# Kernel tuning notes

Hardware: AMD Instinct MI355X
Metric: run time of the kernel (lower is better)

The kernel has to match this reference:

```python
import jax, jax.numpy as jnp
import numpy as np

EPS = 1e-08

def setup_inputs() -> dict:
    key = jax.random.key(0)
    k1, k2, k3 = jax.random.split(key, 3)
    b, cin, cout, ksz, h, w = 16, 256, 256, 3, 64, 64
    return {
        "x": jax.random.normal(k1, (b, cin, h, w), dtype=jnp.float32),
        "s": jax.random.normal(k2, (b, cin), dtype=jnp.float32),
        "weight": jax.random.normal(k3, (cout, cin, ksz, ksz), dtype=jnp.float32),
    }

def reference(x, s, weight):
    # x: [b, cin, h, w]; s: [b, cin]; weight: [cout, cin, k, k]
    b, cin, h, w = x.shape
    cout, _, ksz, _ = weight.shape
    pad = ksz // 2
    # demodulate pre-normalization of weight and style
    wn = weight * jax.lax.rsqrt(jnp.mean(jnp.square(weight), axis=(1, 2, 3), keepdims=True))
    sn = s * jax.lax.rsqrt(jnp.mean(jnp.square(s)))
    # per-sample modulation: [b, cout, cin, k, k]
    wmod = wn[None, :, :, :, :] * sn[:, None, :, None, None]
    # demodulation: normalize each output filter per sample
    sigma_inv = jax.lax.rsqrt(jnp.sum(jnp.square(wmod), axis=(2, 3, 4), keepdims=True) + EPS)
    wmod = wmod * sigma_inv
    # batch-grouped conv: input [1, b*cin, h, w], weight [b*cout, cin, k, k]
    xg = x.reshape(1, b * cin, h, w)
    wg = wmod.reshape(b * cout, cin, ksz, ksz)
    y = jax.lax.conv_general_dilated(
        xg, wg,
        window_strides=(1, 1),
        padding=[(pad, pad), (pad, pad)],
        feature_group_count=b,
        dimension_numbers=("NCHW", "OIHW", "NCHW"),
    )
    return y.reshape(b, cout, h, w)
```

## Files before the change

### kernel.cpp

```cpp
#include <hip/hip_runtime.h>
#include <hip/hip_bf16.h>

#define EPS 1e-8f
#define B_  16
#define CIN 256
#define COUT 256
#define HW 64

typedef __bf16 bf16x8 __attribute__((ext_vector_type(8)));
typedef float  f32x4  __attribute__((ext_vector_type(4)));

__device__ __forceinline__ void async16(void* lds, const void* g) {
    __builtin_amdgcn_global_load_lds(
        (const __attribute__((address_space(1))) unsigned int*)g,
        (__attribute__((address_space(3))) unsigned int*)lds,
        16, 0, 0);
}

__device__ __forceinline__ uint pack2(float lo, float hi) {
    __bf16 a = (__bf16)lo, b = (__bf16)hi;
    unsigned short ua = __builtin_bit_cast(unsigned short, a);
    unsigned short ub = __builtin_bit_cast(unsigned short, b);
    return ((uint)ub << 16) | (uint)ua;
}

__global__ __launch_bounds__(256) void prep_kernel(const float* __restrict__ x,
                                                   const float* __restrict__ s,
                                                   const float* __restrict__ w,
                                                   __bf16* __restrict__ xbf,
                                                   __bf16* __restrict__ wfull,
                                                   __bf16* __restrict__ zrow) {
    __shared__ uint xsd[64 * 160];
    __shared__ float red[8];
    const int bid = blockIdx.x;
    const int t   = threadIdx.x;

    if (bid == 1024) {
        uint4 z = make_uint4(0, 0, 0, 0);
        uint4* zp = (uint4*)zrow;
#pragma unroll
        for (int k = 0; k < 9; ++k) zp[k * 256 + t] = z;
        return;
    }

    if (bid > 1024) {
        const int co = bid - 1025;
        const int ci = t;
        const int lane = t & 63, wid = t >> 6;
        float as = 0.f;
#pragma unroll
        for (int k = 0; k < 16; ++k) { float sv = s[k * 256 + t]; as += sv * sv; }
        const float* wp = w + ((size_t)co * CIN + ci) * 9;
        float wv[9];
        float q = 0.f;
#pragma unroll
        for (int tp = 0; tp < 9; ++tp) { wv[tp] = wp[tp]; q += wv[tp] * wv[tp]; }
        float a = as, qq = q;
        for (int off = 32; off > 0; off >>= 1) {
            a  += __shfl_down(a,  off, 64);
            qq += __shfl_down(qq, off, 64);
        }
        if (lane == 0) { red[wid] = a; red[4 + wid] = qq; }
        __syncthreads();
        const float ssum = red[0] + red[1] + red[2] + red[3];
        const float Sw   = red[4] + red[5] + red[6] + red[7];
        const float sn2  = (float)(B_ * CIN) / ssum;
        const float wn   = rsqrtf(Sw / 2304.f);
        const float wn2sn2 = wn * wn * sn2;
        const float wsn  = wn * sqrtf(sn2);

        for (int b = 0; b < B_; ++b) {
            const float sv = s[b * CIN + ci];
            float v = sv * sv * q;
            for (int off = 32; off > 0; off >>= 1) v += __shfl_down(v, off, 64);
            __syncthreads();
            if (lane == 0) red[wid] = v;
            __syncthreads();
            const float S = red[0] + red[1] + red[2] + red[3];
            const float coef = wsn * rsqrtf(wn2sn2 * S + EPS);
            const float sc = sv * coef;
            const size_t obase = ((size_t)b * 9) * 65536 + (size_t)(ci >> 5) * 8192
                               + (size_t)co * 32 + (ci & 31);
#pragma unroll
            for (int tap = 0; tap < 9; ++tap)
                wfull[obase + (size_t)tap * 65536] = (__bf16)(wv[tap] * sc);
        }
        return;
    }

    const int row = bid & 63;
    const int b   = bid >> 6;
    const float* xbase = x + ((size_t)b * CIN * HW + row) * HW;
#pragma unroll
    for (int k = 0; k < 8; ++k) {
        int p   = k * 256 + t;
        int ci2 = p >> 4;
        int c4  = (p & 15) * 4;
        const float* src = xbase + (size_t)(2 * ci2) * (HW * HW) + c4;
        float4 v0 = *(const float4*)src;
        float4 v1 = *(const float4*)(src + HW * HW);
        const int dj = ci2 + (ci2 >> 2);
#pragma unroll
        for (int i = 0; i < 4; ++i)
            xsd[(c4 + i) * 160 + dj] = pack2((&v0.x)[i], (&v1.x)[i]);
    }
    __syncthreads();
    __bf16* orow = xbf + (((size_t)b * HW + row) * 64) * CIN;
#pragma unroll
    for (int k = 0; k < 8; ++k) {
        int o   = k * 256 + t;
        int col = o >> 5;
        int u   = o & 31;
        const uint* rp = &xsd[col * 160 + 5 * u];
        uint4 vv; vv.x = rp[0]; vv.y = rp[1]; vv.z = rp[2]; vv.w = rp[3];
        *(uint4*)&orow[(size_t)col * CIN + u * 8] = vv;
    }
}

__global__ __launch_bounds__(256, 2) void conv_mfma4(const __bf16* __restrict__ xbf,
                                                     const __bf16* __restrict__ zrow,
                                                     const __bf16* __restrict__ wfull,
                                                     float* __restrict__ out) {
    __shared__ __attribute__((aligned(16))) __bf16 xs[2][1056 * 8];

    const int bid = blockIdx.x;
    const int b   = (bid & 7) + ((bid >= 256) ? 8 : 0);
    const int r0  = ((bid >> 3) & 31) * 2;
    const int t = threadIdx.x;
    const int wy = t >> 6, lane = t & 63;
    const int m16 = lane & 15, q = lane >> 4;

    const __bf16* gsrc[5];
#pragma unroll
    for (int i = 0; i < 5; ++i) {
        int qq, rem;
        if (i < 4) { qq = i;  rem = t; }
        else       { qq = wy; rem = 256 + (lane & 7); }
        int irow = rem / 66;
        int col  = rem - irow * 66;
        int gr   = r0 - 1 + irow;
        if ((unsigned)gr < 64u && col != 0 && col != 65)
            gsrc[i] = xbf + (((size_t)b * HW + gr) * 64 + (col - 1)) * CIN + qq * 8;
        else
            gsrc[i] = zrow + col * CIN + qq * 8;
    }

#pragma unroll
    for (int i = 0; i < 4; ++i)
        async16((char*)xs[0] + (i * 264 + t) * 16, gsrc[i]);
    if (lane < 8)
        async16((char*)xs[0] + (wy * 264 + 256 + lane) * 16, gsrc[4]);

    f32x4 acc[4][8] = {};
    const __bf16* abase = wfull + (size_t)b * 589824
                        + (size_t)(wy * 64 + m16) * 32 + q * 8;

    bf16x8 afc[4];
#pragma unroll
    for (int i = 0; i < 4; ++i)
        afc[i] = *(const bf16x8*)(abase + i * 512);

    for (int cc = 0; cc < 8; ++cc) {
        const __bf16* wb = abase + (size_t)cc * 8192;
        __syncthreads();
        if (cc < 7) {
            const int d = cc * 32 + 32;
#pragma unroll
            for (int i = 0; i < 4; ++i)
                async16((char*)xs[(cc + 1) & 1] + (i * 264 + t) * 16, gsrc[i] + d);
            if (lane < 8)
                async16((char*)xs[(cc + 1) & 1] + (wy * 264 + 256 + lane) * 16, gsrc[4] + d);
        }
        const __bf16* xcur = xs[cc & 1];
#pragma unroll
        for (int tap = 0; tap < 9; ++tap) {
            const int dr = tap / 3, dc = tap % 3;
            bf16x8 bfr[8];
#pragma unroll
            for (int j = 0; j < 8; ++j) {
                const int slot = q * 264 + ((j >> 2) + dr) * 66 + (j & 3) * 16 + m16 + dc;
                bfr[j] = *(const bf16x8*)&xcur[slot * 8];
            }
            bf16x8 afn[4];
            if (tap < 8) {
#pragma unroll
                for (int i = 0; i < 4; ++i)
                    afn[i] = *(const bf16x8*)(wb + (size_t)(tap + 1) * 65536 + i * 512);
            } else if (cc < 7) {
#pragma unroll
                for (int i = 0; i < 4; ++i)
                    afn[i] = *(const bf16x8*)(wb + 8192 + i * 512);
            }
            __builtin_amdgcn_s_setprio(1);
#pragma unroll
            for (int i = 0; i < 4; ++i)
#pragma unroll
                for (int j = 0; j < 8; ++j)
                    acc[i][j] = __builtin_amdgcn_mfma_f32_16x16x32_bf16(afc[i], bfr[j], acc[i][j], 0, 0, 0);
            __builtin_amdgcn_s_setprio(0);
            if (tap < 8 || cc < 7) {
#pragma unroll
                for (int i = 0; i < 4; ++i) afc[i] = afn[i];
            }
        }
    }

#pragma unroll
    for (int i = 0; i < 4; ++i) {
        const int cobase = wy * 64 + i * 16 + q * 4;
#pragma unroll
        for (int reg = 0; reg < 4; ++reg) {
            float* op = out + ((size_t)b * COUT + (cobase + reg)) * (HW * HW) + r0 * HW + m16;
#pragma unroll
            for (int j = 0; j < 8; ++j)
                op[(j >> 2) * HW + (j & 3) * 16] = acc[i][j][reg];
        }
    }
}

extern "C" void kernel_launch(void* const* d_in, const int* in_sizes, int n_in,
                              void* d_out, int out_size, void* d_ws, size_t ws_size,
                              hipStream_t stream) {
    const float* x = (const float*)d_in[0];
    const float* s = (const float*)d_in[1];
    const float* w = (const float*)d_in[2];
    float* out = (float*)d_out;

    float* ws = (float*)d_ws;
    __bf16* wfull = (__bf16*)(ws + 70656);
    __bf16* zrow  = (__bf16*)(ws + 4789248);
    __bf16* xbf   = (__bf16*)(ws + 4798464);

    prep_kernel<<<1281, 256, 0, stream>>>(x, s, w, xbf, wfull, zrow);
    conv_mfma4<<<512, 256, 0, stream>>>(xbf, zrow, wfull, out);
}
```

Baseline: 181.1 us.

## Reuse overlapping conv rows across taps, pad LDS, and use nontemporal loads/stores

```diff
diff --git a/kernel.cpp b/kernel.cpp
--- a/kernel.cpp
+++ b/kernel.cpp
@@ -15,6 +15,12 @@
         (const __attribute__((address_space(1))) unsigned int*)g,
         (__attribute__((address_space(3))) unsigned int*)lds,
         16, 0, 0);
+}
+__device__ __forceinline__ void async16nt(void* lds, const void* g) {
+    __builtin_amdgcn_global_load_lds(
+        (const __attribute__((address_space(1))) unsigned int*)g,
+        (__attribute__((address_space(3))) unsigned int*)lds,
+        16, 0, 2);
 }
 
 __device__ __forceinline__ uint pack2(float lo, float hi) {
@@ -117,11 +123,11 @@
     }
 }
 
-__global__ __launch_bounds__(256, 2) void conv_mfma4(const __bf16* __restrict__ xbf,
+__global__ __launch_bounds__(256, 2) void conv_mfma5(const __bf16* __restrict__ xbf,
                                                      const __bf16* __restrict__ zrow,
                                                      const __bf16* __restrict__ wfull,
                                                      float* __restrict__ out) {
-    __shared__ __attribute__((aligned(16))) __bf16 xs[2][1056 * 8];
+    __shared__ __attribute__((aligned(16))) __bf16 xs[2][1064 * 8];
 
     const int bid = blockIdx.x;
     const int b   = (bid & 7) + ((bid >= 256) ? 8 : 0);
@@ -147,18 +153,15 @@
 
 #pragma unroll
     for (int i = 0; i < 4; ++i)
-        async16((char*)xs[0] + (i * 264 + t) * 16, gsrc[i]);
+        async16nt((char*)xs[0] + (i * 266 + t) * 16, gsrc[i]);
     if (lane < 8)
-        async16((char*)xs[0] + (wy * 264 + 256 + lane) * 16, gsrc[4]);
+        async16nt((char*)xs[0] + (wy * 266 + 256 + lane) * 16, gsrc[4]);
 
     f32x4 acc[4][8] = {};
     const __bf16* abase = wfull + (size_t)b * 589824
                         + (size_t)(wy * 64 + m16) * 32 + q * 8;
 
-    bf16x8 afc[4];
-#pragma unroll
-    for (int i = 0; i < 4; ++i)
-        afc[i] = *(const bf16x8*)(abase + i * 512);
+    const int sbase = q * 266 + m16;
 
     for (int cc = 0; cc < 8; ++cc) {
         const __bf16* wb = abase + (size_t)cc * 8192;
@@ -167,38 +170,52 @@
             const int d = cc * 32 + 32;
 #pragma unroll
             for (int i = 0; i < 4; ++i)
-                async16((char*)xs[(cc + 1) & 1] + (i * 264 + t) * 16, gsrc[i] + d);
+                async16nt((char*)xs[(cc + 1) & 1] + (i * 266 + t) * 16, gsrc[i] + d);
             if (lane < 8)
-                async16((char*)xs[(cc + 1) & 1] + (wy * 264 + 256 + lane) * 16, gsrc[4] + d);
+                async16nt((char*)xs[(cc + 1) & 1] + (wy * 266 + 256 + lane) * 16, gsrc[4] + d);
         }
         const __bf16* xcur = xs[cc & 1];
+
+        bf16x8 afc[4], pb[4];
+#pragma unroll
+        for (int i = 0; i < 4; ++i)
+            afc[i] = *(const bf16x8*)(wb + i * 512);
+#pragma unroll
+        for (int j = 0; j < 4; ++j)
+            pb[j] = *(const bf16x8*)&xcur[(sbase + j * 16) * 8];
+
 #pragma unroll
         for (int tap = 0; tap < 9; ++tap) {
             const int dr = tap / 3, dc = tap % 3;
-            bf16x8 bfr[8];
-#pragma unroll
-            for (int j = 0; j < 8; ++j) {
-                const int slot = q * 264 + ((j >> 2) + dr) * 66 + (j & 3) * 16 + m16 + dc;
-                bfr[j] = *(const bf16x8*)&xcur[slot * 8];
-            }
-            bf16x8 afn[4];
+            bf16x8 cur[4];
+#pragma unroll
+            for (int j = 0; j < 4; ++j)
+                cur[j] = *(const bf16x8*)&xcur[(sbase + (1 + dr) * 66 + j * 16 + dc) * 8];
+            bf16x8 nb[4], afn[4];
             if (tap < 8) {
+                const int ndr = (tap + 1) / 3, ndc = (tap + 1) % 3;
+#pragma unroll
+                for (int j = 0; j < 4; ++j)
+                    nb[j] = *(const bf16x8*)&xcur[(sbase + ndr * 66 + j * 16 + ndc) * 8];
 #pragma unroll
                 for (int i = 0; i < 4; ++i)
                     afn[i] = *(const bf16x8*)(wb + (size_t)(tap + 1) * 65536 + i * 512);
-            } else if (cc < 7) {
-#pragma unroll
-                for (int i = 0; i < 4; ++i)
-                    afn[i] = *(const bf16x8*)(wb + 8192 + i * 512);
             }
             __builtin_amdgcn_s_setprio(1);
 #pragma unroll
-            for (int i = 0; i < 4; ++i)
-#pragma unroll
-                for (int j = 0; j < 8; ++j)
-                    acc[i][j] = __builtin_amdgcn_mfma_f32_16x16x32_bf16(afc[i], bfr[j], acc[i][j], 0, 0, 0);
+            for (int j = 0; j < 4; ++j)
+#pragma unroll
+                for (int i = 0; i < 4; ++i)
+                    acc[i][j] = __builtin_amdgcn_mfma_f32_16x16x32_bf16(afc[i], pb[j], acc[i][j], 0, 0, 0);
+#pragma unroll
+            for (int j = 0; j < 4; ++j)
+#pragma unroll
+                for (int i = 0; i < 4; ++i)
+                    acc[i][4 + j] = __builtin_amdgcn_mfma_f32_16x16x32_bf16(afc[i], cur[j], acc[i][4 + j], 0, 0, 0);
             __builtin_amdgcn_s_setprio(0);
-            if (tap < 8 || cc < 7) {
+            if (tap < 8) {
+#pragma unroll
+                for (int j = 0; j < 4; ++j) pb[j] = nb[j];
 #pragma unroll
                 for (int i = 0; i < 4; ++i) afc[i] = afn[i];
             }
@@ -213,7 +230,7 @@
             float* op = out + ((size_t)b * COUT + (cobase + reg)) * (HW * HW) + r0 * HW + m16;
 #pragma unroll
             for (int j = 0; j < 8; ++j)
-                op[(j >> 2) * HW + (j & 3) * 16] = acc[i][j][reg];
+                __builtin_nontemporal_store(acc[i][j][reg], op + (j >> 2) * HW + (j & 3) * 16);
         }
     }
 }
@@ -232,5 +249,5 @@
     __bf16* xbf   = (__bf16*)(ws + 4798464);
 
     prep_kernel<<<1281, 256, 0, stream>>>(x, s, w, xbf, wfull, zrow);
-    conv_mfma4<<<512, 256, 0, stream>>>(xbf, zrow, wfull, out);
-}
+    conv_mfma5<<<512, 256, 0, stream>>>(xbf, zrow, wfull, out);
+}
```

After: 197.1 us. +8.9%, slower.
